# Performance work log

Hardware: AMD Instinct MI355X
Metric: run time of the kernel (lower is better)

Reference implementation:

```python
import jax, jax.numpy as jnp
import numpy as np

B, U = 64, 512            # batch, max_units
AE = 1024
UE = 256                  # unit_embedding_size
A = 256                   # target_head_attention_size


def setup_inputs() -> dict:
    key = jax.random.key(0)
    ks = jax.random.split(key, 10)
    return {
        "autoregressive_embedding": jax.random.normal(ks[0], (B, U, AE), jnp.float32),
        "own_unit_embeddings": jax.random.normal(ks[1], (B, U, UE), jnp.float32),
        "enemy_unit_embeddings": jax.random.normal(ks[2], (B, U, UE), jnp.float32),
        "nr_own_units": jax.random.randint(ks[3], (B, 1), 0, U).astype(jnp.int64),
        "nr_units_enemy": jax.random.randint(ks[4], (B, 1), 0, U).astype(jnp.int64),
        "nr_own_flags": jax.random.randint(ks[5], (B, 1), 0, 8).astype(jnp.int64),
        "Wq": jax.random.normal(ks[6], (UE + AE, A), jnp.float32) * (1.0 / np.sqrt(UE + AE)),
        "bq": jnp.zeros((A,), jnp.float32),
        "Wk": jax.random.normal(ks[7], (UE, A), jnp.float32) * (1.0 / np.sqrt(UE)),
        "bk": jnp.zeros((A,), jnp.float32),
    }


def reference(autoregressive_embedding, own_unit_embeddings, enemy_unit_embeddings,
              nr_own_units, nr_units_enemy, nr_own_flags, Wq, bq, Wk, bk):
    # combined: [B, U, AE+UE]
    combined = jnp.concatenate([autoregressive_embedding, own_unit_embeddings], axis=2)
    queries = combined @ Wq + bq                       # [B, U, A]
    keys = enemy_unit_embeddings @ Wk + bk             # [B, U, A]
    attention = jnp.einsum("bqd,bkd->bqk", queries, keys) / (A ** 0.5)  # [B, U, U]
    # Vectorized mask: rows in [nr_own_flags, nr_own_units), cols in [0, nr_units_enemy)
    idx = jnp.arange(U)
    row_ok = (idx[None, :] >= nr_own_flags) & (idx[None, :] < nr_own_units)  # [B, U]
    col_ok = idx[None, :] < nr_units_enemy                                   # [B, U]
    mask = jnp.where(row_ok[:, :, None] & col_ok[:, None, :], 1.0, 1e-9)     # [B, U, U]
    return jax.nn.softmax(attention * mask, axis=-1)
```

## Files before the change

### kernel.cpp

```cpp
#include <hip/hip_runtime.h>

constexpr int B  = 64;
constexpr int U  = 512;
constexpr int AE = 1024;
constexpr int UE = 256;
constexpr int A  = 256;
constexpr int KQ = AE + UE;

typedef _Float16 f16x8 __attribute__((ext_vector_type(8)));
typedef float    f32x4 __attribute__((ext_vector_type(4)));

__device__ __forceinline__ void cp16(void* lds, const void* g) {
    __builtin_amdgcn_global_load_lds(
        (const __attribute__((address_space(1))) void*)g,
        (__attribute__((address_space(3))) void*)lds, 16, 0, 0);
}

__global__ void prep(const float* __restrict__ Wq, const float* __restrict__ Wk,
                     _Float16* __restrict__ WqT, _Float16* __restrict__ WkT) {
    int idx = blockIdx.x * 256 + threadIdx.x;
    if (idx < KQ * A) {
        int k = idx >> 8, n = idx & 255;
        WqT[(size_t)n * KQ + k] = (_Float16)Wq[idx];
    } else {
        int j = idx - KQ * A;
        if (j < A * A) {
            int k = j >> 8, n = j & 255;
            WkT[(size_t)n * A + k] = (_Float16)Wk[j];
        }
    }
}

__global__ __launch_bounds__(512) void gemm(
    const float* __restrict__ A1, int s1, int split,
    const float* __restrict__ A2, int s2,
    const _Float16* __restrict__ BT,
    const float* __restrict__ bias,
    _Float16* __restrict__ Out,
    int Ktot)
{
    __shared__ __align__(16) _Float16 Al[2][64][32];
    __shared__ __align__(16) _Float16 Bl[2][256][32];

    const int t    = threadIdx.x;
    const int lane = t & 63;
    const int w    = t >> 6;
    const int mbase = blockIdx.x * 64;

    const int wm = (w & 1) * 32;
    const int wn = (w >> 1) * 64;

    f32x4 acc[2][4] = {};

    const int ar  = t >> 3;
    const int aq  = t & 7;
    const int ap  = aq >> 2;
    const int aq8 = (aq & 3) * 8;
    const size_t grow = mbase + ar;

    const int nk = Ktot >> 6;
    for (int kb = 0; kb < nk; kb++) {
        const int k0 = kb * 64;
        __syncthreads();
        #pragma unroll
        for (int rnd = 0; rnd < 4; rnd++) {
            int s = rnd * 512 + t;
            int p = s >> 10;
            int n = (s & 1023) >> 2;
            int q = s & 3;
            cp16((char*)&Bl[0][0][0] + (size_t)s * 16,
                 BT + (size_t)n * Ktot + (k0 + p * 32 + q * 8));
        }
        {
            int kg = k0 + aq * 8;
            const float* src = (kg < split) ? (A1 + grow * (size_t)s1 + kg)
                                            : (A2 + grow * (size_t)s2 + (kg - split));
            const float4 x = *(const float4*)src;
            const float4 y = *(const float4*)(src + 4);
            f16x8 hv;
            hv[0] = (_Float16)x.x; hv[1] = (_Float16)x.y;
            hv[2] = (_Float16)x.z; hv[3] = (_Float16)x.w;
            hv[4] = (_Float16)y.x; hv[5] = (_Float16)y.y;
            hv[6] = (_Float16)y.z; hv[7] = (_Float16)y.w;
            *(f16x8*)(&Al[ap][ar][aq8]) = hv;
        }
        __syncthreads();
        #pragma unroll
        for (int p = 0; p < 2; p++) {
            f16x8 af[2], bf[4];
            #pragma unroll
            for (int mt = 0; mt < 2; mt++)
                af[mt] = *(const f16x8*)(&Al[p][wm + mt * 16 + (lane & 15)][(lane >> 4) * 8]);
            #pragma unroll
            for (int nt = 0; nt < 4; nt++)
                bf[nt] = *(const f16x8*)(&Bl[p][wn + nt * 16 + (lane & 15)][(lane >> 4) * 8]);
            #pragma unroll
            for (int mt = 0; mt < 2; mt++)
                #pragma unroll
                for (int nt = 0; nt < 4; nt++)
                    acc[mt][nt] = __builtin_amdgcn_mfma_f32_16x16x32_f16(
                        af[mt], bf[nt], acc[mt][nt], 0, 0, 0);
        }
    }
    const int col0 = wn + (lane & 15);
    const int rsub = (lane >> 4) * 4;
    #pragma unroll
    for (int nt = 0; nt < 4; nt++) {
        const int col = col0 + nt * 16;
        const float bv = bias[col];
        #pragma unroll
        for (int mt = 0; mt < 2; mt++)
            #pragma unroll
            for (int r = 0; r < 4; r++) {
                int row = mbase + wm + mt * 16 + rsub + r;
                Out[(size_t)row * 256 + col] = (_Float16)(acc[mt][nt][r] + bv);
            }
    }
}

__global__ __launch_bounds__(256) void attn(
    const _Float16* __restrict__ Qh, const _Float16* __restrict__ Kh,
    const int* __restrict__ nr_own_units, const int* __restrict__ nr_units_enemy,
    const int* __restrict__ nr_own_flags, float* __restrict__ Out)
{
    __shared__ __align__(16) char smem[81920];
    _Float16 (*Kl)[512][32] = (_Float16(*)[512][32])smem;
    _Float16 (*Ql)[32][32]  = (_Float16(*)[32][32])(smem + 65536);
    float (*S)[516] = (float(*)[516])smem;

    const int t    = threadIdx.x;
    const int lane = t & 63;
    const int w    = t >> 6;
    const int b    = blockIdx.y;
    const int qbase = blockIdx.x * 32;

    const int nf = nr_own_flags[b];
    const int nu = nr_own_units[b];
    const int ne = nr_units_enemy[b];

    const _Float16* Qb = Qh + ((size_t)b * 512 + qbase) * 256;
    #pragma unroll
    for (int rnd = 0; rnd < 4; rnd++) {
        int s = rnd * 256 + t;
        int p = s >> 7;
        int row = (s & 127) >> 2;
        int q = s & 3;
        cp16((char*)(smem + 65536) + (size_t)s * 16,
             Qb + (size_t)row * 256 + p * 32 + q * 8);
    }

    f32x4 acc[2][8] = {};
    const _Float16* Kb = Kh + (size_t)b * 512 * 256;
    const int wn = w * 128;

    for (int c = 0; c < 4; c++) {
        __syncthreads();
        #pragma unroll
        for (int rnd = 0; rnd < 16; rnd++) {
            int s = rnd * 256 + t;
            int p = s >> 11;
            int row = (s & 2047) >> 2;
            int q = s & 3;
            cp16(smem + (size_t)s * 16,
                 Kb + (size_t)row * 256 + c * 64 + p * 32 + q * 8);
        }
        __syncthreads();
        #pragma unroll
        for (int p = 0; p < 2; p++) {
            f16x8 af[2], bf[8];
            #pragma unroll
            for (int mt = 0; mt < 2; mt++)
                af[mt] = *(const f16x8*)(&Ql[c * 2 + p][mt * 16 + (lane & 15)][(lane >> 4) * 8]);
            #pragma unroll
            for (int nt = 0; nt < 8; nt++)
                bf[nt] = *(const f16x8*)(&Kl[p][wn + nt * 16 + (lane & 15)][(lane >> 4) * 8]);
            #pragma unroll
            for (int mt = 0; mt < 2; mt++)
                #pragma unroll
                for (int nt = 0; nt < 8; nt++)
                    acc[mt][nt] = __builtin_amdgcn_mfma_f32_16x16x32_f16(
                        af[mt], bf[nt], acc[mt][nt], 0, 0, 0);
        }
    }

    __syncthreads();
    const int rsub = (lane >> 4) * 4;
    #pragma unroll
    for (int nt = 0; nt < 8; nt++) {
        const int col = wn + nt * 16 + (lane & 15);
        const bool cok = col < ne;
        #pragma unroll
        for (int mt = 0; mt < 2; mt++)
            #pragma unroll
            for (int r = 0; r < 4; r++) {
                int row = mt * 16 + rsub + r;
                int uq = qbase + row;
                bool ok = cok && (uq >= nf) && (uq < nu);
                S[row][col] = acc[mt][nt][r] * 0.0625f * (ok ? 1.0f : 1e-9f);
            }
    }
    __syncthreads();

    for (int rr = 0; rr < 8; rr++) {
        const int row = w * 8 + rr;
        float v[8], m = -1e30f;
        #pragma unroll
        for (int i = 0; i < 8; i++) { v[i] = S[row][lane + i * 64]; m = fmaxf(m, v[i]); }
        #pragma unroll
        for (int off = 32; off >= 1; off >>= 1) m = fmaxf(m, __shfl_xor(m, off));
        float e[8], sum = 0.f;
        #pragma unroll
        for (int i = 0; i < 8; i++) { e[i] = __expf(v[i] - m); sum += e[i]; }
        #pragma unroll
        for (int off = 32; off >= 1; off >>= 1) sum += __shfl_xor(sum, off);
        const float inv = 1.0f / sum;
        float* orow = Out + ((size_t)b * 512 + qbase + row) * 512;
        #pragma unroll
        for (int i = 0; i < 8; i++) orow[lane + i * 64] = e[i] * inv;
    }
}

extern "C" void kernel_launch(void* const* d_in, const int* in_sizes, int n_in,
                              void* d_out, int out_size, void* d_ws, size_t ws_size,
                              hipStream_t stream) {
    const float* ar    = (const float*)d_in[0];
    const float* own   = (const float*)d_in[1];
    const float* enemy = (const float*)d_in[2];
    const int*   n_own   = (const int*)d_in[3];
    const int*   n_enemy = (const int*)d_in[4];
    const int*   n_flags = (const int*)d_in[5];
    const float* Wq = (const float*)d_in[6];
    const float* bq = (const float*)d_in[7];
    const float* Wk = (const float*)d_in[8];
    const float* bk = (const float*)d_in[9];
    float* out = (float*)d_out;

    char* ws = (char*)d_ws;
    _Float16* WqT = (_Float16*)(ws);
    _Float16* WkT = (_Float16*)(ws + 655360);
    _Float16* Qh  = (_Float16*)(ws + 786432);
    _Float16* Kh  = (_Float16*)(ws + 786432 + 16777216);

    prep<<<dim3((KQ * A + A * A) / 256), dim3(256), 0, stream>>>(Wq, Wk, WqT, WkT);

    gemm<<<dim3(512), dim3(512), 0, stream>>>(ar, AE, AE, own, UE, WqT, bq, Qh, KQ);
    gemm<<<dim3(512), dim3(512), 0, stream>>>(nullptr, 0, 0, enemy, UE, WkT, bk, Kh, A);

    attn<<<dim3(16, B), dim3(256), 0, stream>>>(Qh, Kh, n_own, n_enemy, n_flags, out);
}
```

Baseline: 345.2 us.

## Register-prefetch GEMM/attn tiles, swizzle LDS, reblock Q/K layout, register softmax

The GEMM replaces direct global-to-LDS copies with register prefetch of the next K tile, overlapping loads with MFMA compute. It also XOR-swizzles LDS columns to reduce bank conflicts. Q and K outputs are written in a column-blocked [b][k/32][u][32] layout so the attention kernel can stream contiguous 32-wide chunks. The attention kernel now uses 64-row tiles with 512 threads and does the masked softmax directly in registers with cross-wave LDS reductions, removing the full score matrix staged in LDS. The risks are higher register pressure and strided 16-lane output stores.

```diff
diff --git a/kernel.cpp b/kernel.cpp
--- a/kernel.cpp
+++ b/kernel.cpp
@@ -9,12 +9,6 @@
 
 typedef _Float16 f16x8 __attribute__((ext_vector_type(8)));
 typedef float    f32x4 __attribute__((ext_vector_type(4)));
-
-__device__ __forceinline__ void cp16(void* lds, const void* g) {
-    __builtin_amdgcn_global_load_lds(
-        (const __attribute__((address_space(1))) void*)g,
-        (__attribute__((address_space(3))) void*)lds, 16, 0, 0);
-}
 
 __global__ void prep(const float* __restrict__ Wq, const float* __restrict__ Wk,
                      _Float16* __restrict__ WqT, _Float16* __restrict__ WkT) {
@@ -55,45 +49,64 @@
     const int ar  = t >> 3;
     const int aq  = t & 7;
     const int ap  = aq >> 2;
-    const int aq8 = (aq & 3) * 8;
+    const int asw = ((aq & 3) ^ ((ar >> 1) & 3)) * 8;
     const size_t grow = mbase + ar;
 
+    int bp[4], bn[4], bq[4], bsw[4];
+    #pragma unroll
+    for (int j = 0; j < 4; j++) {
+        int s = j * 512 + t;
+        bp[j] = s >> 10;
+        bn[j] = (s & 1023) >> 2;
+        bq[j] = s & 3;
+        bsw[j] = ((bq[j] ^ ((bn[j] >> 1) & 3))) * 8;
+    }
+
+    float4 areg0, areg1;
+    f16x8 breg[4];
+
+    auto loadA = [&](int k0) {
+        int kg = k0 + aq * 8;
+        const float* src = (kg < split) ? (A1 + grow * (size_t)s1 + kg)
+                                        : (A2 + grow * (size_t)s2 + (kg - split));
+        areg0 = ((const float4*)src)[0];
+        areg1 = ((const float4*)src)[1];
+    };
+    auto loadB = [&](int k0) {
+        #pragma unroll
+        for (int j = 0; j < 4; j++)
+            breg[j] = *(const f16x8*)(BT + (size_t)bn[j] * Ktot + k0 + bp[j] * 32 + bq[j] * 8);
+    };
+
+    loadA(0);
+    loadB(0);
+
+    const int rsw = (((lane & 15) >> 1) & 3);
     const int nk = Ktot >> 6;
     for (int kb = 0; kb < nk; kb++) {
-        const int k0 = kb * 64;
         __syncthreads();
-        #pragma unroll
-        for (int rnd = 0; rnd < 4; rnd++) {
-            int s = rnd * 512 + t;
-            int p = s >> 10;
-            int n = (s & 1023) >> 2;
-            int q = s & 3;
-            cp16((char*)&Bl[0][0][0] + (size_t)s * 16,
-                 BT + (size_t)n * Ktot + (k0 + p * 32 + q * 8));
-        }
         {
-            int kg = k0 + aq * 8;
-            const float* src = (kg < split) ? (A1 + grow * (size_t)s1 + kg)
-                                            : (A2 + grow * (size_t)s2 + (kg - split));
-            const float4 x = *(const float4*)src;
-            const float4 y = *(const float4*)(src + 4);
             f16x8 hv;
-            hv[0] = (_Float16)x.x; hv[1] = (_Float16)x.y;
-            hv[2] = (_Float16)x.z; hv[3] = (_Float16)x.w;
-            hv[4] = (_Float16)y.x; hv[5] = (_Float16)y.y;
-            hv[6] = (_Float16)y.z; hv[7] = (_Float16)y.w;
-            *(f16x8*)(&Al[ap][ar][aq8]) = hv;
+            hv[0] = (_Float16)areg0.x; hv[1] = (_Float16)areg0.y;
+            hv[2] = (_Float16)areg0.z; hv[3] = (_Float16)areg0.w;
+            hv[4] = (_Float16)areg1.x; hv[5] = (_Float16)areg1.y;
+            hv[6] = (_Float16)areg1.z; hv[7] = (_Float16)areg1.w;
+            *(f16x8*)(&Al[ap][ar][asw]) = hv;
+            #pragma unroll
+            for (int j = 0; j < 4; j++)
+                *(f16x8*)(&Bl[bp[j]][bn[j]][bsw[j]]) = breg[j];
         }
         __syncthreads();
+        if (kb + 1 < nk) { loadA(kb * 64 + 64); loadB(kb * 64 + 64); }
         #pragma unroll
         for (int p = 0; p < 2; p++) {
             f16x8 af[2], bf[4];
             #pragma unroll
             for (int mt = 0; mt < 2; mt++)
-                af[mt] = *(const f16x8*)(&Al[p][wm + mt * 16 + (lane & 15)][(lane >> 4) * 8]);
+                af[mt] = *(const f16x8*)(&Al[p][wm + mt * 16 + (lane & 15)][(((lane >> 4) ^ rsw)) * 8]);
             #pragma unroll
             for (int nt = 0; nt < 4; nt++)
-                bf[nt] = *(const f16x8*)(&Bl[p][wn + nt * 16 + (lane & 15)][(lane >> 4) * 8]);
+                bf[nt] = *(const f16x8*)(&Bl[p][wn + nt * 16 + (lane & 15)][(((lane >> 4) ^ rsw)) * 8]);
             #pragma unroll
             for (int mt = 0; mt < 2; mt++)
                 #pragma unroll
@@ -108,116 +121,176 @@
     for (int nt = 0; nt < 4; nt++) {
         const int col = col0 + nt * 16;
         const float bv = bias[col];
+        const int c5 = col >> 5, c31 = col & 31;
         #pragma unroll
         for (int mt = 0; mt < 2; mt++)
             #pragma unroll
             for (int r = 0; r < 4; r++) {
                 int row = mbase + wm + mt * 16 + rsub + r;
-                Out[(size_t)row * 256 + col] = (_Float16)(acc[mt][nt][r] + bv);
+                int bb = row >> 9, u = row & 511;
+                Out[(((size_t)bb * 8 + c5) * 512 + u) * 32 + c31] =
+                    (_Float16)(acc[mt][nt][r] + bv);
             }
     }
 }
 
-__global__ __launch_bounds__(256) void attn(
+__global__ __launch_bounds__(512) void attn(
     const _Float16* __restrict__ Qh, const _Float16* __restrict__ Kh,
     const int* __restrict__ nr_own_units, const int* __restrict__ nr_units_enemy,
     const int* __restrict__ nr_own_flags, float* __restrict__ Out)
 {
-    __shared__ __align__(16) char smem[81920];
-    _Float16 (*Kl)[512][32] = (_Float16(*)[512][32])smem;
-    _Float16 (*Ql)[32][32]  = (_Float16(*)[32][32])(smem + 65536);
-    float (*S)[516] = (float(*)[516])smem;
+    __shared__ __align__(16) _Float16 Ql[8][64][32];
+    __shared__ __align__(16) _Float16 Kl[512][32];
+    __shared__ float red[64][4];
 
     const int t    = threadIdx.x;
     const int lane = t & 63;
     const int w    = t >> 6;
     const int b    = blockIdx.y;
-    const int qbase = blockIdx.x * 32;
+    const int qbase = blockIdx.x * 64;
 
     const int nf = nr_own_flags[b];
     const int nu = nr_own_units[b];
     const int ne = nr_units_enemy[b];
 
-    const _Float16* Qb = Qh + ((size_t)b * 512 + qbase) * 256;
-    #pragma unroll
-    for (int rnd = 0; rnd < 4; rnd++) {
-        int s = rnd * 256 + t;
-        int p = s >> 7;
-        int row = (s & 127) >> 2;
-        int q = s & 3;
-        cp16((char*)(smem + 65536) + (size_t)s * 16,
-             Qb + (size_t)row * 256 + p * 32 + q * 8);
-    }
+    const int wm = (w & 1) * 32;
+    const int wn = (w >> 1) * 128;
+
+    f16x8 qreg[4];
+    {
+        const _Float16* Qb = Qh + ((size_t)b * 8 * 512 + qbase) * 32;
+        #pragma unroll
+        for (int j = 0; j < 4; j++) {
+            int s = j * 512 + t;
+            int p = s >> 8, row = (s & 255) >> 2, cq = s & 3;
+            qreg[j] = *(const f16x8*)(Qb + ((size_t)p * 512 + row) * 32 + cq * 8);
+        }
+        #pragma unroll
+        for (int j = 0; j < 4; j++) {
+            int s = j * 512 + t;
+            int p = s >> 8, row = (s & 255) >> 2, cq = s & 3;
+            *(f16x8*)(&Ql[p][row][(cq ^ ((row >> 1) & 3)) * 8]) = qreg[j];
+        }
+    }
+
+    const _Float16* Kb = Kh + (size_t)b * 8 * 512 * 32;
+    f16x8 kreg[4];
+    const int krow = t >> 2;
+    const int kq   = t & 3;
+    auto loadK = [&](int c) {
+        const _Float16* Kc = Kb + (size_t)c * 512 * 32;
+        #pragma unroll
+        for (int j = 0; j < 4; j++)
+            kreg[j] = *(const f16x8*)(Kc + ((size_t)(j * 128 + krow)) * 32 + kq * 8);
+    };
+    loadK(0);
 
     f32x4 acc[2][8] = {};
-    const _Float16* Kb = Kh + (size_t)b * 512 * 256;
-    const int wn = w * 128;
-
-    for (int c = 0; c < 4; c++) {
+    const int rsw = (((lane & 15) >> 1) & 3);
+    for (int c = 0; c < 8; c++) {
         __syncthreads();
         #pragma unroll
-        for (int rnd = 0; rnd < 16; rnd++) {
-            int s = rnd * 256 + t;
-            int p = s >> 11;
-            int row = (s & 2047) >> 2;
-            int q = s & 3;
-            cp16(smem + (size_t)s * 16,
-                 Kb + (size_t)row * 256 + c * 64 + p * 32 + q * 8);
+        for (int j = 0; j < 4; j++) {
+            int row = j * 128 + krow;
+            *(f16x8*)(&Kl[row][(kq ^ ((row >> 1) & 3)) * 8]) = kreg[j];
         }
         __syncthreads();
-        #pragma unroll
-        for (int p = 0; p < 2; p++) {
-            f16x8 af[2], bf[8];
-            #pragma unroll
-            for (int mt = 0; mt < 2; mt++)
-                af[mt] = *(const f16x8*)(&Ql[c * 2 + p][mt * 16 + (lane & 15)][(lane >> 4) * 8]);
+        if (c < 7) loadK(c + 1);
+        f16x8 af[2], bf[8];
+        #pragma unroll
+        for (int mt = 0; mt < 2; mt++)
+            af[mt] = *(const f16x8*)(&Ql[c][wm + mt * 16 + (lane & 15)][((lane >> 4) ^ rsw) * 8]);
+        #pragma unroll
+        for (int nt = 0; nt < 8; nt++)
+            bf[nt] = *(const f16x8*)(&Kl[wn + nt * 16 + (lane & 15)][((lane >> 4) ^ rsw) * 8]);
+        #pragma unroll
+        for (int mt = 0; mt < 2; mt++)
             #pragma unroll
             for (int nt = 0; nt < 8; nt++)
-                bf[nt] = *(const f16x8*)(&Kl[p][wn + nt * 16 + (lane & 15)][(lane >> 4) * 8]);
-            #pragma unroll
-            for (int mt = 0; mt < 2; mt++)
-                #pragma unroll
-                for (int nt = 0; nt < 8; nt++)
-                    acc[mt][nt] = __builtin_amdgcn_mfma_f32_16x16x32_f16(
-                        af[mt], bf[nt], acc[mt][nt], 0, 0, 0);
-        }
-    }
-
+                acc[mt][nt] = __builtin_amdgcn_mfma_f32_16x16x32_f16(
+                    af[mt], bf[nt], acc[mt][nt], 0, 0, 0);
+    }
+
+    const int rsub = (lane >> 4) * 4;
+    #pragma unroll
+    for (int mt = 0; mt < 2; mt++)
+        #pragma unroll
+        for (int nt = 0; nt < 8; nt++)
+            #pragma unroll
+            for (int r = 0; r < 4; r++) {
+                int rl = wm + mt * 16 + rsub + r;
+                int uq = qbase + rl;
+                int col = wn + nt * 16 + (lane & 15);
+                bool ok = (col < ne) && (uq >= nf) && (uq < nu);
+                acc[mt][nt][r] = acc[mt][nt][r] * 0.0625f * (ok ? 1.0f : 1e-9f);
+            }
+
+    float mx[2][4];
+    #pragma unroll
+    for (int mt = 0; mt < 2; mt++)
+        #pragma unroll
+        for (int r = 0; r < 4; r++) {
+            float m = acc[mt][0][r];
+            #pragma unroll
+            for (int nt = 1; nt < 8; nt++) m = fmaxf(m, acc[mt][nt][r]);
+            #pragma unroll
+            for (int off = 1; off <= 8; off <<= 1) m = fmaxf(m, __shfl_xor(m, off));
+            mx[mt][r] = m;
+        }
+    if ((lane & 15) == 0) {
+        #pragma unroll
+        for (int mt = 0; mt < 2; mt++)
+            #pragma unroll
+            for (int r = 0; r < 4; r++)
+                red[wm + mt * 16 + rsub + r][w >> 1] = mx[mt][r];
+    }
     __syncthreads();
-    const int rsub = (lane >> 4) * 4;
-    #pragma unroll
-    for (int nt = 0; nt < 8; nt++) {
-        const int col = wn + nt * 16 + (lane & 15);
-        const bool cok = col < ne;
-        #pragma unroll
-        for (int mt = 0; mt < 2; mt++)
-            #pragma unroll
-            for (int r = 0; r < 4; r++) {
-                int row = mt * 16 + rsub + r;
-                int uq = qbase + row;
-                bool ok = cok && (uq >= nf) && (uq < nu);
-                S[row][col] = acc[mt][nt][r] * 0.0625f * (ok ? 1.0f : 1e-9f);
+    #pragma unroll
+    for (int mt = 0; mt < 2; mt++)
+        #pragma unroll
+        for (int r = 0; r < 4; r++) {
+            f32x4 v = *(const f32x4*)(&red[wm + mt * 16 + rsub + r][0]);
+            mx[mt][r] = fmaxf(fmaxf(v[0], v[1]), fmaxf(v[2], v[3]));
+        }
+    __syncthreads();
+
+    float sm[2][4];
+    #pragma unroll
+    for (int mt = 0; mt < 2; mt++)
+        #pragma unroll
+        for (int r = 0; r < 4; r++) {
+            float s = 0.f;
+            #pragma unroll
+            for (int nt = 0; nt < 8; nt++) {
+                float e = __expf(acc[mt][nt][r] - mx[mt][r]);
+                acc[mt][nt][r] = e;
+                s += e;
             }
+            #pragma unroll
+            for (int off = 1; off <= 8; off <<= 1) s += __shfl_xor(s, off);
+            sm[mt][r] = s;
+        }
+    if ((lane & 15) == 0) {
+        #pragma unroll
+        for (int mt = 0; mt < 2; mt++)
+            #pragma unroll
+            for (int r = 0; r < 4; r++)
+                red[wm + mt * 16 + rsub + r][w >> 1] = sm[mt][r];
     }
     __syncthreads();
 
-    for (int rr = 0; rr < 8; rr++) {
-        const int row = w * 8 + rr;
-        float v[8], m = -1e30f;
-        #pragma unroll
-        for (int i = 0; i < 8; i++) { v[i] = S[row][lane + i * 64]; m = fmaxf(m, v[i]); }
-        #pragma unroll
-        for (int off = 32; off >= 1; off >>= 1) m = fmaxf(m, __shfl_xor(m, off));
-        float e[8], sum = 0.f;
-        #pragma unroll
-        for (int i = 0; i < 8; i++) { e[i] = __expf(v[i] - m); sum += e[i]; }
-        #pragma unroll
-        for (int off = 32; off >= 1; off >>= 1) sum += __shfl_xor(sum, off);
-        const float inv = 1.0f / sum;
-        float* orow = Out + ((size_t)b * 512 + qbase + row) * 512;
-        #pragma unroll
-        for (int i = 0; i < 8; i++) orow[lane + i * 64] = e[i] * inv;
-    }
+    #pragma unroll
+    for (int mt = 0; mt < 2; mt++)
+        #pragma unroll
+        for (int r = 0; r < 4; r++) {
+            int rl = wm + mt * 16 + rsub + r;
+            f32x4 v = *(const f32x4*)(&red[rl][0]);
+            float inv = 1.0f / (v[0] + v[1] + v[2] + v[3]);
+            float* orow = Out + ((size_t)b * 512 + qbase + rl) * 512 + wn + (lane & 15);
+            #pragma unroll
+            for (int nt = 0; nt < 8; nt++)
+                orow[nt * 16] = acc[mt][nt][r] * inv;
+        }
 }
 
 extern "C" void kernel_launch(void* const* d_in, const int* in_sizes, int n_in,
@@ -244,7 +317,7 @@
     prep<<<dim3((KQ * A + A * A) / 256), dim3(256), 0, stream>>>(Wq, Wk, WqT, WkT);
 
     gemm<<<dim3(512), dim3(512), 0, stream>>>(ar, AE, AE, own, UE, WqT, bq, Qh, KQ);
-    gemm<<<dim3(512), dim3(512), 0, stream>>>(nullptr, 0, 0, enemy, UE, WkT, bk, Kh, A);
-
-    attn<<<dim3(16, B), dim3(256), 0, stream>>>(Qh, Kh, n_own, n_enemy, n_flags, out);
+    gemm<<<dim3(512), dim3(512), 0, stream>>>(enemy, UE, 0, enemy, UE, WkT, bk, Kh, A);
+
+    attn<<<dim3(8, B), dim3(512), 0, stream>>>(Qh, Kh, n_own, n_enemy, n_flags, out);
 }
```

After: 331.4 us. 4.0% less time.
